# Kernel optimization log

Hardware: AMD Instinct MI355X
Metric: run time of the kernel (lower is better)

Reference implementation:

```python
import jax, jax.numpy as jnp
import numpy as np

D_MODEL = 1024
N_HEADS = 16
HEAD_DIM = D_MODEL // N_HEADS


def setup_inputs() -> dict:
    key = jax.random.key(0)
    ks = jax.random.split(key, 5)
    x = jax.random.normal(ks[0], (4, 2048, D_MODEL), dtype=jnp.float32)
    # Linear params (torch Linear: y = x @ W.T + b); store W as [in, out] for einsum.
    s_in = 1.0 / np.sqrt(D_MODEL)
    w_in = jax.random.uniform(ks[1], (D_MODEL, 3 * D_MODEL), jnp.float32, -s_in, s_in)
    b_in = jax.random.uniform(ks[2], (3 * D_MODEL,), jnp.float32, -s_in, s_in)
    w_out = jax.random.uniform(ks[3], (D_MODEL, D_MODEL), jnp.float32, -s_in, s_in)
    b_out = jax.random.uniform(ks[4], (D_MODEL,), jnp.float32, -s_in, s_in)
    return {"x": x, "w_in": w_in, "b_in": b_in, "w_out": w_out, "b_out": b_out}


def reference(x, w_in, b_in, w_out, b_out):
    B, L, D = x.shape
    H, Hd = N_HEADS, HEAD_DIM
    qkv = jnp.einsum('bld,de->ble', x, w_in) + b_in  # [B,L,3D]
    q, k, v = jnp.split(qkv, 3, axis=-1)
    # [B,H,L,Hd]
    q = q.reshape(B, L, H, Hd).transpose(0, 2, 1, 3)
    k = k.reshape(B, L, H, Hd).transpose(0, 2, 1, 3)
    v = v.reshape(B, L, H, Hd).transpose(0, 2, 1, 3)
    scale = 1.0 / np.sqrt(Hd).astype(np.float32)
    scores = jnp.einsum('bhqd,bhkd->bhqk', q, k) * scale  # [B,H,L,L]
    causal = jnp.tril(jnp.ones((L, L), dtype=bool))
    scores = jnp.where(causal, scores, jnp.finfo(scores.dtype).min)
    attn = jax.nn.softmax(scores, axis=-1)
    out = jnp.einsum('bhqk,bhkd->bhqd', attn, v)  # [B,H,L,Hd]
    out = out.transpose(0, 2, 1, 3).reshape(B, L, D)
    return jnp.einsum('bld,de->ble', out, w_out) + b_out
```

## Files before the change

### kernel.cpp

```cpp
#include <hip/hip_runtime.h>

typedef float f32x4 __attribute__((ext_vector_type(4)));
typedef __bf16 bf16x8 __attribute__((ext_vector_type(8)));
typedef short s16x8 __attribute__((ext_vector_type(8)));
typedef int i32x4 __attribute__((ext_vector_type(4)));

__device__ __forceinline__ unsigned short f2bf(float f) {
  union { float f; unsigned u; } v;
  v.f = f;
  unsigned r = v.u + 0x7FFFu + ((v.u >> 16) & 1u);
  return (unsigned short)(r >> 16);
}

__device__ __forceinline__ int pk2bf(float lo, float hi) {
  unsigned a = __builtin_bit_cast(unsigned, lo) + 0x8000u;
  unsigned b = __builtin_bit_cast(unsigned, hi) + 0x8000u;
  return (int)__builtin_amdgcn_perm(b, a, 0x07060302u);
}

#if __has_builtin(__builtin_amdgcn_exp2f)
__device__ __forceinline__ float fexp2(float x) { return __builtin_amdgcn_exp2f(x); }
#else
__device__ __forceinline__ float fexp2(float x) { return exp2f(x); }
#endif

__device__ __forceinline__ void gl_lds16(const void* g, void* l) {
  __builtin_amdgcn_global_load_lds(
      (__attribute__((address_space(1))) void*)g,
      (__attribute__((address_space(3))) void*)l, 16, 0, 0);
}

__global__ __launch_bounds__(256) void k_convert_x(const float* __restrict__ in,
                                                   short* __restrict__ out) {
  int i = (blockIdx.x * 256 + threadIdx.x) * 8;
  const float4* p = (const float4*)(in + i);
  float4 a = p[0], b = p[1];
  s16x8 r;
  r[0] = (short)f2bf(a.x); r[1] = (short)f2bf(a.y);
  r[2] = (short)f2bf(a.z); r[3] = (short)f2bf(a.w);
  r[4] = (short)f2bf(b.x); r[5] = (short)f2bf(b.y);
  r[6] = (short)f2bf(b.z); r[7] = (short)f2bf(b.w);
  *(s16x8*)(out + i) = r;
}

__global__ __launch_bounds__(256) void k_transpose_cvt(const float* __restrict__ in,
                                                       short* __restrict__ out,
                                                       int R, int C) {
  __shared__ short tile[32][33];
  int c0 = blockIdx.x * 32, r0 = blockIdx.y * 32;
  int tx = threadIdx.x, ty = threadIdx.y;
#pragma unroll
  for (int i = 0; i < 32; i += 8)
    tile[ty + i][tx] = (short)f2bf(in[(size_t)(r0 + ty + i) * C + c0 + tx]);
  __syncthreads();
#pragma unroll
  for (int i = 0; i < 32; i += 8)
    out[(size_t)(c0 + ty + i) * R + r0 + tx] = tile[tx][ty + i];
}

__global__ __launch_bounds__(256) void k_qkv_gemm(const short* __restrict__ A,
                                                  const short* __restrict__ B,
                                                  const float* __restrict__ bias,
                                                  short* __restrict__ qb,
                                                  short* __restrict__ kb,
                                                  short* __restrict__ vtb) {
  __shared__ short As[128 * 32];
  __shared__ short Bs[128 * 32];
  const int tid = threadIdx.x;
  const int lane = tid & 63;
  const int w = tid >> 6;
  const int g = lane >> 4, c = lane & 15;
  const int m0 = blockIdx.y * 128, n0 = blockIdx.x * 128;
  const int wm = (w >> 1) * 64, wn = (w & 1) * 64;
  f32x4 acc[4][4] = {};
  const int p0 = tid, p1 = tid + 256;
  const int rowA0 = p0 >> 2, logA0 = (p0 & 3) ^ ((p0 >> 3) & 3);
  const int rowA1 = p1 >> 2, logA1 = (p1 & 3) ^ ((p1 >> 3) & 3);
  const short* a0 = A + (size_t)(m0 + rowA0) * 1024 + logA0 * 8;
  const short* a1 = A + (size_t)(m0 + rowA1) * 1024 + logA1 * 8;
  const short* b0 = B + (size_t)(n0 + rowA0) * 1024 + logA0 * 8;
  const short* b1 = B + (size_t)(n0 + rowA1) * 1024 + logA1 * 8;
  short* lA0 = As + p0 * 8; short* lA1 = As + p1 * 8;
  short* lB0 = Bs + p0 * 8; short* lB1 = Bs + p1 * 8;

  for (int k0 = 0; k0 < 1024; k0 += 32) {
    gl_lds16(a0 + k0, lA0);
    gl_lds16(a1 + k0, lA1);
    gl_lds16(b0 + k0, lB0);
    gl_lds16(b1 + k0, lB1);
    __syncthreads();
    bf16x8 af[4], bfr[4];
#pragma unroll
    for (int t = 0; t < 4; t++) {
      int ra = wm + t * 16 + c;
      af[t] = *(const bf16x8*)(As + ra * 32 + (g ^ ((ra >> 1) & 3)) * 8);
      int rb = wn + t * 16 + c;
      bfr[t] = *(const bf16x8*)(Bs + rb * 32 + (g ^ ((rb >> 1) & 3)) * 8);
    }
#pragma unroll
    for (int i = 0; i < 4; i++)
#pragma unroll
      for (int jn = 0; jn < 4; jn++)
        acc[i][jn] = __builtin_amdgcn_mfma_f32_16x16x32_bf16(af[i], bfr[jn], acc[i][jn], 0, 0, 0);
    __syncthreads();
  }

  const int which = n0 >> 10;
  const float qscale = 0.125f * 1.4426950408889634f;
  if (which == 2) {
#pragma unroll
    for (int jn = 0; jn < 4; jn++) {
      const int col = n0 + wn + jn * 16 + c;
      const float bv = bias[col];
      const int cw = col & 1023;
      const int h = cw >> 6, d = cw & 63;
#pragma unroll
      for (int i = 0; i < 4; i++) {
        const int row = m0 + wm + i * 16 + g * 4;
        const int bb = row >> 11, l0 = row & 2047;
        int lo = pk2bf(acc[i][jn][0] + bv, acc[i][jn][1] + bv);
        int hi = pk2bf(acc[i][jn][2] + bv, acc[i][jn][3] + bv);
        *(int2*)(vtb + (size_t)((bb * 16 + h) * 64 + d) * 2048 + l0) = make_int2(lo, hi);
      }
    }
  } else {
    short* dst = (which == 0) ? qb : kb;
    const float sc = (which == 0) ? qscale : 1.0f;
#pragma unroll
    for (int jn = 0; jn < 4; jn++) {
      const int col = n0 + wn + jn * 16 + c;
      const float bv = bias[col];
      const int cw = col & 1023;
      const int h = cw >> 6, d = cw & 63;
#pragma unroll
      for (int i = 0; i < 4; i++) {
#pragma unroll
        for (int r = 0; r < 4; r++) {
          const int row = m0 + wm + i * 16 + g * 4 + r;
          const int bb = row >> 11, l = row & 2047;
          dst[((size_t)((bb * 16 + h) * 2048 + l) << 6) + d] = (short)f2bf((acc[i][jn][r] + bv) * sc);
        }
      }
    }
  }
}

__device__ __forceinline__ int sigma_row(int rho) {
  return ((rho >> 5) << 5) | (((rho >> 2) & 3) << 3) | (((rho >> 4) & 1) << 2) | (rho & 3);
}

__device__ __forceinline__ void stage_kv512(const short* __restrict__ Kt,
                                            const short* __restrict__ Vtt,
                                            short* ksb, short* vsb, int tid) {
#pragma unroll
  for (int t = 0; t < 2; t++) {
    int p = tid + t * 512;
    int krow = p >> 3, kchk = (p & 7) ^ (krow & 7);
    gl_lds16(Kt + (size_t)sigma_row(krow) * 64 + kchk * 8, ksb + p * 8);
    int dv = p >> 4, vchk = (p & 15) ^ (dv & 15);
    gl_lds16(Vtt + (size_t)dv * 2048 + vchk * 8, vsb + p * 8);
  }
}

__global__ __launch_bounds__(512, 2) void k_attn(const short* __restrict__ Q,
                                                 const short* __restrict__ K,
                                                 const short* __restrict__ Vt,
                                                 short* __restrict__ O) {
  __shared__ short Ks[2][128 * 64];
  __shared__ short Vs[2][64 * 128];
  const int tid = threadIdx.x;
  const int lane = tid & 63;
  const int w = tid >> 6;
  const int quad = lane >> 4, cq = lane & 15;
  const int bh = blockIdx.y;
  const int bb = bh >> 4, h = bh & 15;
  const size_t base = (size_t)bh * (2048 * 64);
  const int pr = blockIdx.x;
  const int qhi = 15 - pr, qlo = pr;
  const int jmax = qhi;
  const int qloc = w * 16 + cq;

  bf16x8 qf[2][2];
#pragma unroll
  for (int mt = 0; mt < 2; mt++) {
    const int qt = mt ? qlo : qhi;
#pragma unroll
    for (int kd = 0; kd < 2; kd++)
      qf[mt][kd] = *(const bf16x8*)(Q + base +
          (size_t)(qt * 128 + w * 16 + cq) * 64 + (kd * 4 + quad) * 8);
  }

  stage_kv512(K + base, Vt + base, Ks[0], Vs[0], tid);

  f32x4 o[2][4] = {};
  float m_run[2] = {-1e30f, -1e30f};
  float l_run[2] = {0.f, 0.f};

  for (int j = 0; j <= jmax; j++) {
    const int cur = j & 1;
    __syncthreads();
    if (j < jmax)
      stage_kv512(K + base + (size_t)(j + 1) * 128 * 64, Vt + base + (j + 1) * 128,
                  Ks[cur ^ 1], Vs[cur ^ 1], tid);
    const short* ks = Ks[cur];
    const short* vs = Vs[cur];
    const bool act1 = (j <= qlo);

    f32x4 s[2][8] = {};
    if (act1) {
#pragma unroll
      for (int kd = 0; kd < 2; kd++)
#pragma unroll
        for (int nt = 0; nt < 8; nt++) {
          int krow = nt * 16 + cq;
          bf16x8 kf = *(const bf16x8*)(ks + krow * 64 + ((kd * 4 + quad) ^ (krow & 7)) * 8);
          s[0][nt] = __builtin_amdgcn_mfma_f32_16x16x32_bf16(kf, qf[0][kd], s[0][nt], 0, 0, 0);
          s[1][nt] = __builtin_amdgcn_mfma_f32_16x16x32_bf16(kf, qf[1][kd], s[1][nt], 0, 0, 0);
        }
    } else {
#pragma unroll
      for (int kd = 0; kd < 2; kd++)
#pragma unroll
        for (int nt = 0; nt < 8; nt++) {
          int krow = nt * 16 + cq;
          bf16x8 kf = *(const bf16x8*)(ks + krow * 64 + ((kd * 4 + quad) ^ (krow & 7)) * 8);
          s[0][nt] = __builtin_amdgcn_mfma_f32_16x16x32_bf16(kf, qf[0][kd], s[0][nt], 0, 0, 0);
        }
    }

    bf16x8 pf[2][4];
    const int nmt = act1 ? 2 : 1;
#pragma unroll
    for (int mt = 0; mt < 2; mt++) {
      if (mt >= nmt) break;
      const bool diag = (j == (mt ? qlo : qhi));
      float mx = -1e30f;
      if (diag) {
#pragma unroll
        for (int nt = 0; nt < 8; nt++)
#pragma unroll
          for (int r = 0; r < 4; r++) {
            int key = (nt >> 1) * 32 + (nt & 1) * 4 + r;
            float v = (key + quad * 8 > qloc) ? -1e30f : s[mt][nt][r];
            s[mt][nt][r] = v;
            mx = fmaxf(mx, v);
          }
      } else {
#pragma unroll
        for (int nt = 0; nt < 8; nt++)
#pragma unroll
          for (int r = 0; r < 4; r++) mx = fmaxf(mx, s[mt][nt][r]);
      }
      mx = fmaxf(mx, __shfl_xor(mx, 16));
      mx = fmaxf(mx, __shfl_xor(mx, 32));
      const float mn = fmaxf(m_run[mt], mx);
      const float alpha = fexp2(m_run[mt] - mn);
      m_run[mt] = mn;
      float lt = 0.f;
#pragma unroll
      for (int nt = 0; nt < 8; nt++)
#pragma unroll
        for (int r = 0; r < 4; r++) {
          float p = fexp2(s[mt][nt][r] - mn);
          s[mt][nt][r] = p;
          lt += p;
        }
      l_run[mt] = l_run[mt] * alpha + lt;
#pragma unroll
      for (int dn = 0; dn < 4; dn++) o[mt][dn] *= alpha;
#pragma unroll
      for (int kt = 0; kt < 4; kt++) {
        i32x4 ow;
        ow[0] = pk2bf(s[mt][2 * kt][0], s[mt][2 * kt][1]);
        ow[1] = pk2bf(s[mt][2 * kt][2], s[mt][2 * kt][3]);
        ow[2] = pk2bf(s[mt][2 * kt + 1][0], s[mt][2 * kt + 1][1]);
        ow[3] = pk2bf(s[mt][2 * kt + 1][2], s[mt][2 * kt + 1][3]);
        pf[mt][kt] = __builtin_bit_cast(bf16x8, ow);
      }
    }

    if (act1) {
#pragma unroll
      for (int kt = 0; kt < 4; kt++)
#pragma unroll
        for (int dn = 0; dn < 4; dn++) {
          int drow = dn * 16 + cq;
          bf16x8 vtf = *(const bf16x8*)(vs + drow * 128 + ((kt * 4 + quad) ^ (drow & 15)) * 8);
          o[0][dn] = __builtin_amdgcn_mfma_f32_16x16x32_bf16(vtf, pf[0][kt], o[0][dn], 0, 0, 0);
          o[1][dn] = __builtin_amdgcn_mfma_f32_16x16x32_bf16(vtf, pf[1][kt], o[1][dn], 0, 0, 0);
        }
    } else {
#pragma unroll
      for (int kt = 0; kt < 4; kt++)
#pragma unroll
        for (int dn = 0; dn < 4; dn++) {
          int drow = dn * 16 + cq;
          bf16x8 vtf = *(const bf16x8*)(vs + drow * 128 + ((kt * 4 + quad) ^ (drow & 15)) * 8);
          o[0][dn] = __builtin_amdgcn_mfma_f32_16x16x32_bf16(vtf, pf[0][kt], o[0][dn], 0, 0, 0);
        }
    }
  }

#pragma unroll
  for (int mt = 0; mt < 2; mt++) {
    const int qt = mt ? qlo : qhi;
    float lf = l_run[mt];
    lf += __shfl_xor(lf, 16);
    lf += __shfl_xor(lf, 32);
    const float inv = 1.f / lf;
    const size_t rb = ((size_t)(bb * 2048 + qt * 128 + w * 16 + cq)) * 1024 + h * 64;
#pragma unroll
    for (int dn = 0; dn < 4; dn++) {
      int d0 = pk2bf(o[mt][dn][0] * inv, o[mt][dn][1] * inv);
      int d1 = pk2bf(o[mt][dn][2] * inv, o[mt][dn][3] * inv);
      *(int2*)(O + rb + dn * 16 + quad * 4) = make_int2(d0, d1);
    }
  }
}

__global__ __launch_bounds__(256) void k_out_gemm(const short* __restrict__ A,
                                                  const short* __restrict__ B,
                                                  const float* __restrict__ bias,
                                                  float* __restrict__ out) {
  __shared__ short As[128 * 32];
  __shared__ short Bs[128 * 32];
  const int tid = threadIdx.x;
  const int lane = tid & 63;
  const int w = tid >> 6;
  const int g = lane >> 4, c = lane & 15;
  const int m0 = blockIdx.y * 128, n0 = blockIdx.x * 128;
  const int wm = (w >> 1) * 64, wn = (w & 1) * 64;
  f32x4 acc[4][4] = {};
  const int p0 = tid, p1 = tid + 256;
  const int rowA0 = p0 >> 2, logA0 = (p0 & 3) ^ ((p0 >> 3) & 3);
  const int rowA1 = p1 >> 2, logA1 = (p1 & 3) ^ ((p1 >> 3) & 3);
  const short* a0 = A + (size_t)(m0 + rowA0) * 1024 + logA0 * 8;
  const short* a1 = A + (size_t)(m0 + rowA1) * 1024 + logA1 * 8;
  const short* b0 = B + (size_t)(n0 + rowA0) * 1024 + logA0 * 8;
  const short* b1 = B + (size_t)(n0 + rowA1) * 1024 + logA1 * 8;
  short* lA0 = As + p0 * 8; short* lA1 = As + p1 * 8;
  short* lB0 = Bs + p0 * 8; short* lB1 = Bs + p1 * 8;

  for (int k0 = 0; k0 < 1024; k0 += 32) {
    gl_lds16(a0 + k0, lA0);
    gl_lds16(a1 + k0, lA1);
    gl_lds16(b0 + k0, lB0);
    gl_lds16(b1 + k0, lB1);
    __syncthreads();
    bf16x8 af[4], bfr[4];
#pragma unroll
    for (int t = 0; t < 4; t++) {
      int ra = wm + t * 16 + c;
      af[t] = *(const bf16x8*)(As + ra * 32 + (g ^ ((ra >> 1) & 3)) * 8);
      int rb = wn + t * 16 + c;
      bfr[t] = *(const bf16x8*)(Bs + rb * 32 + (g ^ ((rb >> 1) & 3)) * 8);
    }
#pragma unroll
    for (int i = 0; i < 4; i++)
#pragma unroll
      for (int jn = 0; jn < 4; jn++)
        acc[i][jn] = __builtin_amdgcn_mfma_f32_16x16x32_bf16(af[i], bfr[jn], acc[i][jn], 0, 0, 0);
    __syncthreads();
  }
#pragma unroll
  for (int jn = 0; jn < 4; jn++) {
    const int col = n0 + wn + jn * 16 + c;
    const float bv = bias[col];
#pragma unroll
    for (int i = 0; i < 4; i++) {
#pragma unroll
      for (int r = 0; r < 4; r++) {
        const int row = m0 + wm + i * 16 + g * 4 + r;
        out[(size_t)row * 1024 + col] = acc[i][jn][r] + bv;
      }
    }
  }
}

extern "C" void kernel_launch(void* const* d_in, const int* in_sizes, int n_in,
                              void* d_out, int out_size, void* d_ws, size_t ws_size,
                              hipStream_t stream) {
  const float* x     = (const float*)d_in[0];
  const float* w_in  = (const float*)d_in[1];
  const float* b_in  = (const float*)d_in[2];
  const float* w_out = (const float*)d_in[3];
  const float* b_out = (const float*)d_in[4];
  float* out = (float*)d_out;
  char* ws = (char*)d_ws;
  short* x_bf   = (short*)(ws);
  short* w_inT  = (short*)(ws + (16ull << 20));
  short* w_outT = (short*)(ws + (22ull << 20));
  short* qb     = (short*)(ws + (24ull << 20));
  short* kb     = (short*)(ws + (40ull << 20));
  short* vtb    = (short*)(ws + (56ull << 20));
  short* ao     = (short*)(ws + (72ull << 20));

  k_convert_x<<<dim3(4096), dim3(256), 0, stream>>>(x, x_bf);
  k_transpose_cvt<<<dim3(96, 32), dim3(32, 8), 0, stream>>>(w_in, w_inT, 1024, 3072);
  k_transpose_cvt<<<dim3(32, 32), dim3(32, 8), 0, stream>>>(w_out, w_outT, 1024, 1024);
  k_qkv_gemm<<<dim3(24, 64), dim3(256), 0, stream>>>(x_bf, w_inT, b_in, qb, kb, vtb);
  k_attn<<<dim3(8, 64), dim3(512), 0, stream>>>(qb, kb, vtb, ao);
  k_out_gemm<<<dim3(8, 64), dim3(256), 0, stream>>>(ao, w_outT, b_out, out);
}
```

Before: 276.1 us.

## Double-buffer GEMM LDS tiles, use hardware bf16 pack, max3 and setprio

Both GEMM kernels now stage the next K-tile into a second LDS buffer while MFMAs run on the current one, with one barrier per iteration instead of two. Bf16 packing switches from the add-and-perm trick to the native v_cvt_pk_bf16_f32 instruction, which rounds to nearest even instead of half-up. The attention row max is computed with v_max3_f32 trees. MFMA sections are wrapped in s_setprio so waves doing matrix work are favoured. LDS use doubles in the GEMMs, which could lower occupancy.

```diff
diff --git a/kernel.cpp b/kernel.cpp
--- a/kernel.cpp
+++ b/kernel.cpp
@@ -12,10 +12,16 @@
   return (unsigned short)(r >> 16);
 }
 
-__device__ __forceinline__ int pk2bf(float lo, float hi) {
-  unsigned a = __builtin_bit_cast(unsigned, lo) + 0x8000u;
-  unsigned b = __builtin_bit_cast(unsigned, hi) + 0x8000u;
-  return (int)__builtin_amdgcn_perm(b, a, 0x07060302u);
+__device__ __forceinline__ int cvt_pk_bf16(float lo, float hi) {
+  int d;
+  asm("v_cvt_pk_bf16_f32 %0, %1, %2" : "=v"(d) : "v"(lo), "v"(hi));
+  return d;
+}
+
+__device__ __forceinline__ float max3f(float a, float b, float c) {
+  float d;
+  asm("v_max3_f32 %0, %1, %2, %3" : "=v"(d) : "v"(a), "v"(b), "v"(c));
+  return d;
 }
 
 #if __has_builtin(__builtin_amdgcn_exp2f)
@@ -64,8 +70,8 @@
                                                   short* __restrict__ qb,
                                                   short* __restrict__ kb,
                                                   short* __restrict__ vtb) {
-  __shared__ short As[128 * 32];
-  __shared__ short Bs[128 * 32];
+  __shared__ short As[2][128 * 32];
+  __shared__ short Bs[2][128 * 32];
   const int tid = threadIdx.x;
   const int lane = tid & 63;
   const int w = tid >> 6;
@@ -80,29 +86,35 @@
   const short* a1 = A + (size_t)(m0 + rowA1) * 1024 + logA1 * 8;
   const short* b0 = B + (size_t)(n0 + rowA0) * 1024 + logA0 * 8;
   const short* b1 = B + (size_t)(n0 + rowA1) * 1024 + logA1 * 8;
-  short* lA0 = As + p0 * 8; short* lA1 = As + p1 * 8;
-  short* lB0 = Bs + p0 * 8; short* lB1 = Bs + p1 * 8;
-
+
+  auto stage = [&](int k0, int buf) {
+    gl_lds16(a0 + k0, As[buf] + p0 * 8);
+    gl_lds16(a1 + k0, As[buf] + p1 * 8);
+    gl_lds16(b0 + k0, Bs[buf] + p0 * 8);
+    gl_lds16(b1 + k0, Bs[buf] + p1 * 8);
+  };
+
+  stage(0, 0);
+  int cur = 0;
   for (int k0 = 0; k0 < 1024; k0 += 32) {
-    gl_lds16(a0 + k0, lA0);
-    gl_lds16(a1 + k0, lA1);
-    gl_lds16(b0 + k0, lB0);
-    gl_lds16(b1 + k0, lB1);
     __syncthreads();
+    if (k0 + 32 < 1024) stage(k0 + 32, cur ^ 1);
+    const short* as = As[cur];
+    const short* bs = Bs[cur];
     bf16x8 af[4], bfr[4];
 #pragma unroll
     for (int t = 0; t < 4; t++) {
       int ra = wm + t * 16 + c;
-      af[t] = *(const bf16x8*)(As + ra * 32 + (g ^ ((ra >> 1) & 3)) * 8);
+      af[t] = *(const bf16x8*)(as + ra * 32 + (g ^ ((ra >> 1) & 3)) * 8);
       int rb = wn + t * 16 + c;
-      bfr[t] = *(const bf16x8*)(Bs + rb * 32 + (g ^ ((rb >> 1) & 3)) * 8);
+      bfr[t] = *(const bf16x8*)(bs + rb * 32 + (g ^ ((rb >> 1) & 3)) * 8);
     }
 #pragma unroll
     for (int i = 0; i < 4; i++)
 #pragma unroll
       for (int jn = 0; jn < 4; jn++)
         acc[i][jn] = __builtin_amdgcn_mfma_f32_16x16x32_bf16(af[i], bfr[jn], acc[i][jn], 0, 0, 0);
-    __syncthreads();
+    cur ^= 1;
   }
 
   const int which = n0 >> 10;
@@ -118,8 +130,8 @@
       for (int i = 0; i < 4; i++) {
         const int row = m0 + wm + i * 16 + g * 4;
         const int bb = row >> 11, l0 = row & 2047;
-        int lo = pk2bf(acc[i][jn][0] + bv, acc[i][jn][1] + bv);
-        int hi = pk2bf(acc[i][jn][2] + bv, acc[i][jn][3] + bv);
+        int lo = cvt_pk_bf16(acc[i][jn][0] + bv, acc[i][jn][1] + bv);
+        int hi = cvt_pk_bf16(acc[i][jn][2] + bv, acc[i][jn][3] + bv);
         *(int2*)(vtb + (size_t)((bb * 16 + h) * 64 + d) * 2048 + l0) = make_int2(lo, hi);
       }
     }
@@ -207,6 +219,7 @@
     const bool act1 = (j <= qlo);
 
     f32x4 s[2][8] = {};
+    __builtin_amdgcn_s_setprio(1);
     if (act1) {
 #pragma unroll
       for (int kd = 0; kd < 2; kd++)
@@ -227,6 +240,7 @@
           s[0][nt] = __builtin_amdgcn_mfma_f32_16x16x32_bf16(kf, qf[0][kd], s[0][nt], 0, 0, 0);
         }
     }
+    __builtin_amdgcn_s_setprio(0);
 
     bf16x8 pf[2][4];
     const int nmt = act1 ? 2 : 1;
@@ -234,25 +248,27 @@
     for (int mt = 0; mt < 2; mt++) {
       if (mt >= nmt) break;
       const bool diag = (j == (mt ? qlo : qhi));
-      float mx = -1e30f;
       if (diag) {
 #pragma unroll
         for (int nt = 0; nt < 8; nt++)
 #pragma unroll
           for (int r = 0; r < 4; r++) {
             int key = (nt >> 1) * 32 + (nt & 1) * 4 + r;
-            float v = (key + quad * 8 > qloc) ? -1e30f : s[mt][nt][r];
-            s[mt][nt][r] = v;
-            mx = fmaxf(mx, v);
+            if (key + quad * 8 > qloc) s[mt][nt][r] = -1e30f;
           }
-      } else {
+      }
+      float mx;
+      {
+        float pm[8];
 #pragma unroll
         for (int nt = 0; nt < 8; nt++)
-#pragma unroll
-          for (int r = 0; r < 4; r++) mx = fmaxf(mx, s[mt][nt][r]);
+          pm[nt] = fmaxf(max3f(s[mt][nt][0], s[mt][nt][1], s[mt][nt][2]), s[mt][nt][3]);
+        mx = max3f(max3f(pm[0], pm[1], pm[2]), max3f(pm[3], pm[4], pm[5]),
+                   fmaxf(pm[6], pm[7]));
       }
       mx = fmaxf(mx, __shfl_xor(mx, 16));
       mx = fmaxf(mx, __shfl_xor(mx, 32));
+
       const float mn = fmaxf(m_run[mt], mx);
       const float alpha = fexp2(m_run[mt] - mn);
       m_run[mt] = mn;
@@ -271,14 +287,15 @@
 #pragma unroll
       for (int kt = 0; kt < 4; kt++) {
         i32x4 ow;
-        ow[0] = pk2bf(s[mt][2 * kt][0], s[mt][2 * kt][1]);
-        ow[1] = pk2bf(s[mt][2 * kt][2], s[mt][2 * kt][3]);
-        ow[2] = pk2bf(s[mt][2 * kt + 1][0], s[mt][2 * kt + 1][1]);
-        ow[3] = pk2bf(s[mt][2 * kt + 1][2], s[mt][2 * kt + 1][3]);
+        ow[0] = cvt_pk_bf16(s[mt][2 * kt][0], s[mt][2 * kt][1]);
+        ow[1] = cvt_pk_bf16(s[mt][2 * kt][2], s[mt][2 * kt][3]);
+        ow[2] = cvt_pk_bf16(s[mt][2 * kt + 1][0], s[mt][2 * kt + 1][1]);
+        ow[3] = cvt_pk_bf16(s[mt][2 * kt + 1][2], s[mt][2 * kt + 1][3]);
         pf[mt][kt] = __builtin_bit_cast(bf16x8, ow);
       }
     }
 
+    __builtin_amdgcn_s_setprio(1);
     if (act1) {
 #pragma unroll
       for (int kt = 0; kt < 4; kt++)
@@ -299,6 +316,7 @@
           o[0][dn] = __builtin_amdgcn_mfma_f32_16x16x32_bf16(vtf, pf[0][kt], o[0][dn], 0, 0, 0);
         }
     }
+    __builtin_amdgcn_s_setprio(0);
   }
 
 #pragma unroll
@@ -311,8 +329,8 @@
     const size_t rb = ((size_t)(bb * 2048 + qt * 128 + w * 16 + cq)) * 1024 + h * 64;
 #pragma unroll
     for (int dn = 0; dn < 4; dn++) {
-      int d0 = pk2bf(o[mt][dn][0] * inv, o[mt][dn][1] * inv);
-      int d1 = pk2bf(o[mt][dn][2] * inv, o[mt][dn][3] * inv);
+      int d0 = cvt_pk_bf16(o[mt][dn][0] * inv, o[mt][dn][1] * inv);
+      int d1 = cvt_pk_bf16(o[mt][dn][2] * inv, o[mt][dn][3] * inv);
       *(int2*)(O + rb + dn * 16 + quad * 4) = make_int2(d0, d1);
     }
   }
@@ -322,8 +340,8 @@
                                                   const short* __restrict__ B,
                                                   const float* __restrict__ bias,
                                                   float* __restrict__ out) {
-  __shared__ short As[128 * 32];
-  __shared__ short Bs[128 * 32];
+  __shared__ short As[2][128 * 32];
+  __shared__ short Bs[2][128 * 32];
   const int tid = threadIdx.x;
   const int lane = tid & 63;
   const int w = tid >> 6;
@@ -338,29 +356,35 @@
   const short* a1 = A + (size_t)(m0 + rowA1) * 1024 + logA1 * 8;
   const short* b0 = B + (size_t)(n0 + rowA0) * 1024 + logA0 * 8;
   const short* b1 = B + (size_t)(n0 + rowA1) * 1024 + logA1 * 8;
-  short* lA0 = As + p0 * 8; short* lA1 = As + p1 * 8;
-  short* lB0 = Bs + p0 * 8; short* lB1 = Bs + p1 * 8;
-
+
+  auto stage = [&](int k0, int buf) {
+    gl_lds16(a0 + k0, As[buf] + p0 * 8);
+    gl_lds16(a1 + k0, As[buf] + p1 * 8);
+    gl_lds16(b0 + k0, Bs[buf] + p0 * 8);
+    gl_lds16(b1 + k0, Bs[buf] + p1 * 8);
+  };
+
+  stage(0, 0);
+  int cur = 0;
   for (int k0 = 0; k0 < 1024; k0 += 32) {
-    gl_lds16(a0 + k0, lA0);
-    gl_lds16(a1 + k0, lA1);
-    gl_lds16(b0 + k0, lB0);
-    gl_lds16(b1 + k0, lB1);
     __syncthreads();
+    if (k0 + 32 < 1024) stage(k0 + 32, cur ^ 1);
+    const short* as = As[cur];
+    const short* bs = Bs[cur];
     bf16x8 af[4], bfr[4];
 #pragma unroll
     for (int t = 0; t < 4; t++) {
       int ra = wm + t * 16 + c;
-      af[t] = *(const bf16x8*)(As + ra * 32 + (g ^ ((ra >> 1) & 3)) * 8);
+      af[t] = *(const bf16x8*)(as + ra * 32 + (g ^ ((ra >> 1) & 3)) * 8);
       int rb = wn + t * 16 + c;
-      bfr[t] = *(const bf16x8*)(Bs + rb * 32 + (g ^ ((rb >> 1) & 3)) * 8);
+      bfr[t] = *(const bf16x8*)(bs + rb * 32 + (g ^ ((rb >> 1) & 3)) * 8);
     }
 #pragma unroll
     for (int i = 0; i < 4; i++)
 #pragma unroll
       for (int jn = 0; jn < 4; jn++)
         acc[i][jn] = __builtin_amdgcn_mfma_f32_16x16x32_bf16(af[i], bfr[jn], acc[i][jn], 0, 0, 0);
-    __syncthreads();
+    cur ^= 1;
   }
 #pragma unroll
   for (int jn = 0; jn < 4; jn++) {
```

After: 280.9 us. Within noise of the previous version (+1.7%).

## Merge prep kernels, remap GEMM workgroups per XCD, use hardware bf16 pack and setprio

Applied to the files above, without the earlier changes.

Merges the x conversion and both weight transpose kernels into one launch, which removes two kernel launches and their gaps. Remaps the workgroup IDs in both GEMMs so consecutive tiles land on the same XCD, which should improve L2 reuse. In attention, replaces the manual bf16 packing with the hardware v_cvt_pk_bf16_f32 instruction, computes the row max with v_max3 trees, and wraps the MFMA loops in s_setprio. Several unrelated micro-optimizations are bundled, and the inline asm may limit compiler scheduling.

```diff
diff --git a/kernel.cpp b/kernel.cpp
--- a/kernel.cpp
+++ b/kernel.cpp
@@ -12,10 +12,16 @@
   return (unsigned short)(r >> 16);
 }
 
-__device__ __forceinline__ int pk2bf(float lo, float hi) {
-  unsigned a = __builtin_bit_cast(unsigned, lo) + 0x8000u;
-  unsigned b = __builtin_bit_cast(unsigned, hi) + 0x8000u;
-  return (int)__builtin_amdgcn_perm(b, a, 0x07060302u);
+__device__ __forceinline__ int cvt_pk_bf16(float lo, float hi) {
+  int d;
+  asm("v_cvt_pk_bf16_f32 %0, %1, %2" : "=v"(d) : "v"(lo), "v"(hi));
+  return d;
+}
+
+__device__ __forceinline__ float max3f(float a, float b, float c) {
+  float d;
+  asm("v_max3_f32 %0, %1, %2, %3" : "=v"(d) : "v"(a), "v"(b), "v"(c));
+  return d;
 }
 
 #if __has_builtin(__builtin_amdgcn_exp2f)
@@ -30,25 +36,12 @@
       (__attribute__((address_space(3))) void*)l, 16, 0, 0);
 }
 
-__global__ __launch_bounds__(256) void k_convert_x(const float* __restrict__ in,
-                                                   short* __restrict__ out) {
-  int i = (blockIdx.x * 256 + threadIdx.x) * 8;
-  const float4* p = (const float4*)(in + i);
-  float4 a = p[0], b = p[1];
-  s16x8 r;
-  r[0] = (short)f2bf(a.x); r[1] = (short)f2bf(a.y);
-  r[2] = (short)f2bf(a.z); r[3] = (short)f2bf(a.w);
-  r[4] = (short)f2bf(b.x); r[5] = (short)f2bf(b.y);
-  r[6] = (short)f2bf(b.z); r[7] = (short)f2bf(b.w);
-  *(s16x8*)(out + i) = r;
-}
-
-__global__ __launch_bounds__(256) void k_transpose_cvt(const float* __restrict__ in,
-                                                       short* __restrict__ out,
-                                                       int R, int C) {
+__device__ __forceinline__ void transpose_cvt_body(const float* __restrict__ in,
+                                                   short* __restrict__ out,
+                                                   int R, int C, int bx, int by, int tid) {
   __shared__ short tile[32][33];
-  int c0 = blockIdx.x * 32, r0 = blockIdx.y * 32;
-  int tx = threadIdx.x, ty = threadIdx.y;
+  int c0 = bx * 32, r0 = by * 32;
+  int tx = tid & 31, ty = tid >> 5;
 #pragma unroll
   for (int i = 0; i < 32; i += 8)
     tile[ty + i][tx] = (short)f2bf(in[(size_t)(r0 + ty + i) * C + c0 + tx]);
@@ -56,6 +49,33 @@
 #pragma unroll
   for (int i = 0; i < 32; i += 8)
     out[(size_t)(c0 + ty + i) * R + r0 + tx] = tile[tx][ty + i];
+}
+
+__global__ __launch_bounds__(256) void k_prep(const float* __restrict__ x,
+                                              short* __restrict__ x_bf,
+                                              const float* __restrict__ w_in,
+                                              short* __restrict__ w_inT,
+                                              const float* __restrict__ w_out,
+                                              short* __restrict__ w_outT) {
+  const int bid = blockIdx.x;
+  const int tid = threadIdx.x;
+  if (bid < 4096) {
+    int i = (bid * 256 + tid) * 8;
+    const float4* p = (const float4*)(x + i);
+    float4 a = p[0], b = p[1];
+    s16x8 r;
+    r[0] = (short)f2bf(a.x); r[1] = (short)f2bf(a.y);
+    r[2] = (short)f2bf(a.z); r[3] = (short)f2bf(a.w);
+    r[4] = (short)f2bf(b.x); r[5] = (short)f2bf(b.y);
+    r[6] = (short)f2bf(b.z); r[7] = (short)f2bf(b.w);
+    *(s16x8*)(x_bf + i) = r;
+  } else if (bid < 4096 + 3072) {
+    const int local = bid - 4096;
+    transpose_cvt_body(w_in, w_inT, 1024, 3072, local % 96, local / 96, tid);
+  } else {
+    const int local = bid - (4096 + 3072);
+    transpose_cvt_body(w_out, w_outT, 1024, 1024, local % 32, local / 32, tid);
+  }
 }
 
 __global__ __launch_bounds__(256) void k_qkv_gemm(const short* __restrict__ A,
@@ -70,7 +90,9 @@
   const int lane = tid & 63;
   const int w = tid >> 6;
   const int g = lane >> 4, c = lane & 15;
-  const int m0 = blockIdx.y * 128, n0 = blockIdx.x * 128;
+  const int orig = blockIdx.y * 24 + blockIdx.x;
+  const int wgs = (orig & 7) * 192 + (orig >> 3);
+  const int m0 = (wgs / 24) * 128, n0 = (wgs % 24) * 128;
   const int wm = (w >> 1) * 64, wn = (w & 1) * 64;
   f32x4 acc[4][4] = {};
   const int p0 = tid, p1 = tid + 256;
@@ -118,8 +140,8 @@
       for (int i = 0; i < 4; i++) {
         const int row = m0 + wm + i * 16 + g * 4;
         const int bb = row >> 11, l0 = row & 2047;
-        int lo = pk2bf(acc[i][jn][0] + bv, acc[i][jn][1] + bv);
-        int hi = pk2bf(acc[i][jn][2] + bv, acc[i][jn][3] + bv);
+        int lo = cvt_pk_bf16(acc[i][jn][0] + bv, acc[i][jn][1] + bv);
+        int hi = cvt_pk_bf16(acc[i][jn][2] + bv, acc[i][jn][3] + bv);
         *(int2*)(vtb + (size_t)((bb * 16 + h) * 64 + d) * 2048 + l0) = make_int2(lo, hi);
       }
     }
@@ -207,6 +229,7 @@
     const bool act1 = (j <= qlo);
 
     f32x4 s[2][8] = {};
+    __builtin_amdgcn_s_setprio(1);
     if (act1) {
 #pragma unroll
       for (int kd = 0; kd < 2; kd++)
@@ -227,6 +250,7 @@
           s[0][nt] = __builtin_amdgcn_mfma_f32_16x16x32_bf16(kf, qf[0][kd], s[0][nt], 0, 0, 0);
         }
     }
+    __builtin_amdgcn_s_setprio(0);
 
     bf16x8 pf[2][4];
     const int nmt = act1 ? 2 : 1;
@@ -234,25 +258,27 @@
     for (int mt = 0; mt < 2; mt++) {
       if (mt >= nmt) break;
       const bool diag = (j == (mt ? qlo : qhi));
-      float mx = -1e30f;
       if (diag) {
 #pragma unroll
         for (int nt = 0; nt < 8; nt++)
 #pragma unroll
           for (int r = 0; r < 4; r++) {
             int key = (nt >> 1) * 32 + (nt & 1) * 4 + r;
-            float v = (key + quad * 8 > qloc) ? -1e30f : s[mt][nt][r];
-            s[mt][nt][r] = v;
-            mx = fmaxf(mx, v);
+            if (key + quad * 8 > qloc) s[mt][nt][r] = -1e30f;
           }
-      } else {
+      }
+      float mx;
+      {
+        float pm[8];
 #pragma unroll
         for (int nt = 0; nt < 8; nt++)
-#pragma unroll
-          for (int r = 0; r < 4; r++) mx = fmaxf(mx, s[mt][nt][r]);
+          pm[nt] = fmaxf(max3f(s[mt][nt][0], s[mt][nt][1], s[mt][nt][2]), s[mt][nt][3]);
+        mx = max3f(max3f(pm[0], pm[1], pm[2]), max3f(pm[3], pm[4], pm[5]),
+                   fmaxf(pm[6], pm[7]));
       }
       mx = fmaxf(mx, __shfl_xor(mx, 16));
       mx = fmaxf(mx, __shfl_xor(mx, 32));
+
       const float mn = fmaxf(m_run[mt], mx);
       const float alpha = fexp2(m_run[mt] - mn);
       m_run[mt] = mn;
@@ -271,14 +297,15 @@
 #pragma unroll
       for (int kt = 0; kt < 4; kt++) {
         i32x4 ow;
-        ow[0] = pk2bf(s[mt][2 * kt][0], s[mt][2 * kt][1]);
-        ow[1] = pk2bf(s[mt][2 * kt][2], s[mt][2 * kt][3]);
-        ow[2] = pk2bf(s[mt][2 * kt + 1][0], s[mt][2 * kt + 1][1]);
-        ow[3] = pk2bf(s[mt][2 * kt + 1][2], s[mt][2 * kt + 1][3]);
+        ow[0] = cvt_pk_bf16(s[mt][2 * kt][0], s[mt][2 * kt][1]);
+        ow[1] = cvt_pk_bf16(s[mt][2 * kt][2], s[mt][2 * kt][3]);
+        ow[2] = cvt_pk_bf16(s[mt][2 * kt + 1][0], s[mt][2 * kt + 1][1]);
+        ow[3] = cvt_pk_bf16(s[mt][2 * kt + 1][2], s[mt][2 * kt + 1][3]);
         pf[mt][kt] = __builtin_bit_cast(bf16x8, ow);
       }
     }
 
+    __builtin_amdgcn_s_setprio(1);
     if (act1) {
 #pragma unroll
       for (int kt = 0; kt < 4; kt++)
@@ -299,6 +326,7 @@
           o[0][dn] = __builtin_amdgcn_mfma_f32_16x16x32_bf16(vtf, pf[0][kt], o[0][dn], 0, 0, 0);
         }
     }
+    __builtin_amdgcn_s_setprio(0);
   }
 
 #pragma unroll
@@ -311,8 +339,8 @@
     const size_t rb = ((size_t)(bb * 2048 + qt * 128 + w * 16 + cq)) * 1024 + h * 64;
 #pragma unroll
     for (int dn = 0; dn < 4; dn++) {
-      int d0 = pk2bf(o[mt][dn][0] * inv, o[mt][dn][1] * inv);
-      int d1 = pk2bf(o[mt][dn][2] * inv, o[mt][dn][3] * inv);
+      int d0 = cvt_pk_bf16(o[mt][dn][0] * inv, o[mt][dn][1] * inv);
+      int d1 = cvt_pk_bf16(o[mt][dn][2] * inv, o[mt][dn][3] * inv);
       *(int2*)(O + rb + dn * 16 + quad * 4) = make_int2(d0, d1);
     }
   }
@@ -328,7 +356,9 @@
   const int lane = tid & 63;
   const int w = tid >> 6;
   const int g = lane >> 4, c = lane & 15;
-  const int m0 = blockIdx.y * 128, n0 = blockIdx.x * 128;
+  const int orig = blockIdx.y * 8 + blockIdx.x;
+  const int wgs = (orig & 7) * 64 + (orig >> 3);
+  const int m0 = (wgs >> 3) * 128, n0 = (wgs & 7) * 128;
   const int wm = (w >> 1) * 64, wn = (w & 1) * 64;
   f32x4 acc[4][4] = {};
   const int p0 = tid, p1 = tid + 256;
@@ -395,9 +425,7 @@
   short* vtb    = (short*)(ws + (56ull << 20));
   short* ao     = (short*)(ws + (72ull << 20));
 
-  k_convert_x<<<dim3(4096), dim3(256), 0, stream>>>(x, x_bf);
-  k_transpose_cvt<<<dim3(96, 32), dim3(32, 8), 0, stream>>>(w_in, w_inT, 1024, 3072);
-  k_transpose_cvt<<<dim3(32, 32), dim3(32, 8), 0, stream>>>(w_out, w_outT, 1024, 1024);
+  k_prep<<<dim3(8192), dim3(256), 0, stream>>>(x, x_bf, w_in, w_inT, w_out, w_outT);
   k_qkv_gemm<<<dim3(24, 64), dim3(256), 0, stream>>>(x_bf, w_inT, b_in, qb, kb, vtb);
   k_attn<<<dim3(8, 64), dim3(512), 0, stream>>>(qb, kb, vtb, ao);
   k_out_gemm<<<dim3(8, 64), dim3(256), 0, stream>>>(ao, w_outT, b_out, out);
```

Result: faster. 268.5 us (-2.8%).
